# Optimization experiments

Measured on AMD Instinct MI355X. Metric: run time of the kernel, lower is better.

The kernel has to match this reference:

```python
import jax, jax.numpy as jnp
import numpy as np
from jax import lax

DROPOUT = 0.6  # input dropout rate (recurrent_dropout = 0.0)


def _lstm_layer(x, Wk, Wr, b, drop_key, rate):
    """Keras-style LSTM (gate order i,f,c,o) with per-gate time-constant input dropout.
    x: [B,T,D]; Wk: [D,4U]; Wr: [U,4U]; b: [4U]. Returns (hs [B,T,U], h_last [B,U])."""
    B, T, D = x.shape
    U = Wr.shape[0]
    Wk4 = Wk.reshape(D, 4, U)
    Wr4 = Wr.reshape(U, 4, U)
    b4 = b.reshape(4, U)
    if rate > 0.0:
        keep = 1.0 - rate
        masks = jax.random.bernoulli(drop_key, keep, (4, B, D)).astype(x.dtype) / keep
    else:
        masks = jnp.ones((4, B, D), dtype=x.dtype)

    def step(carry, x_t):
        h, c = carry
        # per-gate dropped inputs: [4,B,D] -> [B,4,U]
        z = jnp.einsum('gbd,dgu->bgu', x_t[None] * masks, Wk4)
        z = z + jnp.einsum('bu,ugv->bgv', h, Wr4) + b4
        i = jax.nn.sigmoid(z[:, 0])
        f = jax.nn.sigmoid(z[:, 1])
        g = jnp.tanh(z[:, 2])
        o = jax.nn.sigmoid(z[:, 3])
        c = f * c + i * g
        h = o * jnp.tanh(c)
        return (h, c), h

    h0 = jnp.zeros((B, U), dtype=x.dtype)
    c0 = jnp.zeros((B, U), dtype=x.dtype)
    (h_last, _), hs = lax.scan(step, (h0, c0), x.transpose(1, 0, 2))
    return hs.transpose(1, 0, 2), h_last


def _glorot(key, shape):
    fan_in, fan_out = shape[0], shape[1]
    scale = jnp.sqrt(2.0 / (fan_in + fan_out)).astype(jnp.float32)
    return jax.random.normal(key, shape, dtype=jnp.float32) * scale


def setup_inputs() -> dict:
    key = jax.random.key(0)
    B, T, D, H, L = 256, 1024, 128, 128, 64
    ks = jax.random.split(key, 10)
    x = jax.random.normal(ks[0], (B, T, D), dtype=jnp.float32)
    return {
        'x': x,
        'Wk0': _glorot(ks[1], (D, 4 * H)), 'Wr0': _glorot(ks[2], (H, 4 * H)),
        'b0': jnp.zeros((4 * H,), jnp.float32),
        'Wk1': _glorot(ks[3], (H, 4 * H)), 'Wr1': _glorot(ks[4], (H, 4 * H)),
        'b1': jnp.zeros((4 * H,), jnp.float32),
        'Wko': _glorot(ks[5], (H, 4 * L)), 'Wro': _glorot(ks[6], (L, 4 * L)),
        'bo': jnp.zeros((4 * L,), jnp.float32),
    }


def reference(x, Wk0, Wr0, b0, Wk1, Wr1, b1, Wko, Wro, bo):
    dk = jax.random.split(jax.random.key(4347), 3)
    h, _ = _lstm_layer(x, Wk0, Wr0, b0, dk[0], DROPOUT)      # hidden layer 0, return_sequences
    h, _ = _lstm_layer(h, Wk1, Wr1, b1, dk[1], DROPOUT)      # hidden layer 1, return_sequences
    _, h_last = _lstm_layer(h, Wko, Wro, bo, dk[2], DROPOUT)  # output layer, last state only
    return h_last
```

## Files before the change

### kernel.cpp

```cpp
#include <hip/hip_runtime.h>
#include <hip/hip_bf16.h>
#include <hip/hip_fp16.h>
#include <stdint.h>


#define MODE_F32  0
#define MODE_F16  2

typedef _Float16 f16x8 __attribute__((ext_vector_type(8)));
typedef float    f32x4 __attribute__((ext_vector_type(4)));

__device__ __forceinline__ float h16f(uint16_t b){
  __half_raw hr; hr.x = b; return __half2float(__half(hr));
}

__device__ __forceinline__ float fexp2(float x){
#if __has_builtin(__builtin_amdgcn_exp2f)
  return __builtin_amdgcn_exp2f(x);
#else
  return exp2f(x);
#endif
}
__device__ __forceinline__ float frcp(float x){
#if __has_builtin(__builtin_amdgcn_rcpf)
  return __builtin_amdgcn_rcpf(x);
#else
  return 1.0f/x;
#endif
}
#define LOG2E  1.4426950408889634f
#define LOG2E2 2.8853900817779268f

template<int M>
__device__ __forceinline__ void cvt8(const void* p, size_t i, float* o){
  if constexpr (M == MODE_F32){
    const float* f = (const float*)p + i;
    float4 a = *(const float4*)f;
    float4 b = *(const float4*)(f + 4);
    o[0]=a.x; o[1]=a.y; o[2]=a.z; o[3]=a.w;
    o[4]=b.x; o[5]=b.y; o[6]=b.z; o[7]=b.w;
  } else {
    uint4 r = *(const uint4*)((const uint16_t*)p + i);
    uint32_t hw[4] = {r.x, r.y, r.z, r.w};
    #pragma unroll
    for (int q=0;q<4;q++){
      o[2*q]   = h16f((uint16_t)(hw[q] & 0xffffu));
      o[2*q+1] = h16f((uint16_t)(hw[q] >> 16));
    }
  }
}

__device__ __forceinline__ void tf2x32(uint32_t k0, uint32_t k1,
                                       uint32_t& x0, uint32_t& x1){
  uint32_t ks2 = k0 ^ k1 ^ 0x1BD11BDAu;
  x0 += k0; x1 += k1;
#define TF_R(r) { x0 += x1; x1 = (x1<<r)|(x1>>(32-r)); x1 ^= x0; }
  TF_R(13) TF_R(15) TF_R(26) TF_R(6)  x0 += k1;  x1 += ks2 + 1u;
  TF_R(17) TF_R(29) TF_R(16) TF_R(24) x0 += ks2; x1 += k0  + 2u;
  TF_R(13) TF_R(15) TF_R(26) TF_R(6)  x0 += k0;  x1 += k1  + 3u;
  TF_R(17) TF_R(29) TF_R(16) TF_R(24) x0 += k1;  x1 += ks2 + 4u;
  TF_R(13) TF_R(15) TF_R(26) TF_R(6)  x0 += ks2; x1 += k0  + 5u;
#undef TF_R
}

__device__ __forceinline__ float bern_mask(uint32_t bits){
  float u = __uint_as_float((bits >> 9) | 0x3f800000u) - 1.0f;
  return (u < 0.4f) ? 2.5f : 0.0f;
}

__global__ void mask_kernel(float* __restrict__ masks){
  int gid = blockIdx.x * 256 + threadIdx.x;
  int layer = gid >> 17;
  uint32_t i = (uint32_t)(gid & 131071);
  uint32_t k0 = 0u, k1 = (uint32_t)layer;
  tf2x32(0u, 4347u, k0, k1);
  uint32_t x0 = 0u, x1 = i;
  tf2x32(k0, k1, x0, x1);
  masks[gid] = bern_mask(x0 ^ x1);
}

template<int U, int AM>
__global__ __launch_bounds__(256) void gemm_mfma(
    const void*  __restrict__ A,
    const float* __restrict__ W,
    const float* __restrict__ bias,
    const float* __restrict__ maskL,
    __half* __restrict__ Z)
{
  constexpr int WC   = 4*U;
  constexpr int HALF = U/2;
  __shared__ _Float16 As [128][128];
  __shared__ _Float16 Bst[U  ][128];
  const int tid  = threadIdx.x;
  const int r0   = blockIdx.x * 128;
  const int gate = blockIdx.y;
  const int bb   = blockIdx.x >> 3;
  const float* mrow = maskL + gate*32768 + bb*128;

  {
    const int r  = tid >> 1;
    const int kh = (tid & 1) * 64;
    #pragma unroll
    for (int c=0;c<8;c++){
      int k0 = kh + c*8;
      float av[8]; cvt8<AM>(A, (size_t)(r0+r)*128 + k0, av);
      float4 m0 = *(const float4*)(mrow+k0);
      float4 m1 = *(const float4*)(mrow+k0+4);
      _Float16* dst = &As[r][k0 ^ ((r&7)<<3)];
      dst[0]=(_Float16)(av[0]*m0.x); dst[1]=(_Float16)(av[1]*m0.y);
      dst[2]=(_Float16)(av[2]*m0.z); dst[3]=(_Float16)(av[3]*m0.w);
      dst[4]=(_Float16)(av[4]*m1.x); dst[5]=(_Float16)(av[5]*m1.y);
      dst[6]=(_Float16)(av[6]*m1.z); dst[7]=(_Float16)(av[7]*m1.w);
    }
  }
  {
    const int d  = tid >> 1;
    const int ch = (tid & 1) * HALF;
    #pragma unroll
    for (int cc=0; cc<HALF/8; ++cc){
      int c0 = ch + cc*8;
      const float* wp = W + (size_t)d*WC + gate*U + c0;
      float4 w0 = *(const float4*)wp;
      float4 w1 = *(const float4*)(wp+4);
      float wv[8] = {w0.x,w0.y,w0.z,w0.w,w1.x,w1.y,w1.z,w1.w};
      #pragma unroll
      for (int q=0;q<8;q++){
        int c = c0 + q;
        Bst[c][d ^ ((c&7)<<3)] = (_Float16)wv[q];
      }
    }
  }
  __syncthreads();

  const int l  = tid & 63;
  const int w  = tid >> 6;
  const int lr = l & 15;
  const int kg = (l >> 4) * 8;
  constexpr int MF = (U==128) ? 4 : 2;
  const int wr = (U==128) ? ((w>>1)*64) : (w*32);
  const int wc = (U==128) ? ((w&1)*64) : 0;

  f32x4 zz = {0.f,0.f,0.f,0.f};
  f32x4 acc[MF][4];
  #pragma unroll
  for (int m=0;m<MF;m++)
    #pragma unroll
    for (int n=0;n<4;n++) acc[m][n] = zz;

  #pragma unroll
  for (int ks=0; ks<4; ++ks){
    const int kb = ks*32 + kg;
    f16x8 af[MF], bf[4];
    #pragma unroll
    for (int m=0;m<MF;m++){
      int r = wr + m*16 + lr;
      af[m] = *(const f16x8*)&As[r][kb ^ ((r&7)<<3)];
    }
    #pragma unroll
    for (int n=0;n<4;n++){
      int c = wc + n*16 + lr;
      bf[n] = *(const f16x8*)&Bst[c][kb ^ ((c&7)<<3)];
    }
    #pragma unroll
    for (int m=0;m<MF;m++)
      #pragma unroll
      for (int n=0;n<4;n++)
        acc[m][n] = __builtin_amdgcn_mfma_f32_16x16x32_f16(af[m], bf[n], acc[m][n], 0, 0, 0);
  }

  const int crow = (l>>4)*4;
  float bv[4];
  #pragma unroll
  for (int n=0;n<4;n++) bv[n] = bias[gate*U + wc + n*16 + lr];
  #pragma unroll
  for (int m=0;m<MF;m++){
    #pragma unroll
    for (int n=0;n<4;n++){
      int cc = wc + n*16 + lr;
      #pragma unroll
      for (int j=0;j<4;j++){
        int rr = wr + m*16 + crow + j;
        Z[(size_t)(r0+rr)*WC + gate*U + cc] = __float2half(acc[m][n][j] + bv[n]);
      }
    }
  }
}

template<int U, bool SEQ, int VAR>
__global__ __launch_bounds__(4*U, 1) void rec5_kernel(
    const __half* __restrict__ Zin,
    const float*  __restrict__ Wr,
    __half* __restrict__ Hseq,
    float*  __restrict__ Hlast)
{
  constexpr int C   = 4*U;
  constexpr int KS  = U/32;
  constexpr int TS  = 32;
  constexpr int TBH = TS*C;
  constexpr int NCH = 4;
  const int row = blockIdx.x;
  const int tid = threadIdx.x;
  const int l   = tid & 63;
  const int w   = tid >> 6;
  const int lr  = l & 15;
  const int kg  = (l >> 4) * 8;
  const int u   = w*16 + lr;

  __shared__ _Float16 zt[2][TBH];
  __shared__ _Float16 hbuf[2][U];

  f16x8 bf[4][KS];
  #pragma unroll
  for (int g=0; g<4; ++g)
    #pragma unroll
    for (int ks=0; ks<KS; ++ks)
      #pragma unroll
      for (int j=0; j<8; ++j)
        bf[g][ks][j] = (_Float16)Wr[(size_t)(ks*32 + kg + j)*C + g*U + u];

  if (tid < U) hbuf[0][tid] = (_Float16)0.0f;
  float cst = 0.0f;

  const char* zrow = (const char*)Zin + (size_t)row*1024*C*2;
  auto stage = [&](int tile, int buf){
    const char* gsrc = zrow + (size_t)tile*TBH*2;
    char* lbase = (char*)&zt[buf][0];
    #pragma unroll
    for (int c=0; c<NCH; ++c){
      int off = c*(4*U*16) + tid*16;
      __builtin_amdgcn_global_load_lds(
          (const uint32_t*)(gsrc + off),
          (uint32_t*)(lbase + c*(4*U*16) + w*1024),
          16, 0, 0);
    }
  };
  stage(0, 0);

  uint16_t* hsq = nullptr;
  if constexpr (SEQ) hsq = (uint16_t*)Hseq + (size_t)row*1024*U + u;

  asm volatile("s_waitcnt vmcnt(0) lgkmcnt(0)" ::: "memory");
  __builtin_amdgcn_s_barrier();

  for (int tile=0; tile<1024/TS; ++tile){
    const int buf = tile & 1;
    if (tile+1 < 1024/TS) stage(tile+1, buf^1);

    #pragma unroll 1
    for (int s8=0; s8<TS/8; ++s8){
      uint16_t hr[8];
      #pragma unroll
      for (int r8=0; r8<8; ++r8){
        const int s  = s8*8 + r8;
        const int tt = tile*TS + s;
        const int hb = r8 & 1;
        f16x8 af[KS];
        #pragma unroll
        for (int ks=0; ks<KS; ++ks)
          af[ks] = *(const f16x8*)&hbuf[hb][ks*32 + kg];
        float zg0 = (float)zt[buf][s*C         + u];
        float zg1 = (float)zt[buf][s*C +   U   + u];
        float zg2 = (float)zt[buf][s*C + 2*U   + u];
        float zg3 = (float)zt[buf][s*C + 3*U   + u];
        f32x4 acc[4];
        acc[0] = (f32x4){zg0,zg0,zg0,zg0};
        acc[1] = (f32x4){zg1,zg1,zg1,zg1};
        acc[2] = (f32x4){zg2,zg2,zg2,zg2};
        acc[3] = (f32x4){zg3,zg3,zg3,zg3};
        #pragma unroll
        for (int g=0; g<4; ++g)
          #pragma unroll
          for (int ks=0; ks<KS; ++ks)
            acc[g] = __builtin_amdgcn_mfma_f32_16x16x32_f16(af[ks], bf[g][ks], acc[g], 0, 0, 0);
        float gi = frcp(1.0f + fexp2(-LOG2E * acc[0][0]));
        float gf = frcp(1.0f + fexp2(-LOG2E * acc[1][0]));
        float gg = 1.0f - 2.0f*frcp(fexp2(LOG2E2 * acc[2][0]) + 1.0f);
        float go = frcp(1.0f + fexp2(-LOG2E * acc[3][0]));
        cst = fmaf(gf, cst, gi*gg);
        float h = go * (1.0f - 2.0f*frcp(fexp2(LOG2E2 * cst) + 1.0f));
        __half hh = __float2half(h);
        hr[r8] = *(uint16_t*)&hh;
        if (l < 16){
          hbuf[hb ^ 1][u] = *(_Float16*)&hh;
          if constexpr (!SEQ){
            if (tt == 1023) Hlast[(size_t)row*U + u] = h;
          }
        }
        if constexpr (VAR == 0){
          __builtin_amdgcn_sched_barrier(0);
          asm volatile("s_waitcnt lgkmcnt(0)");
          __builtin_amdgcn_s_barrier();
          __builtin_amdgcn_sched_barrier(0);
        } else {
          asm volatile("s_waitcnt lgkmcnt(0)\n\ts_barrier" ::: "memory");
        }
      }
      if constexpr (SEQ){
        if (l < 16){
          uint16_t* hp = hsq + (size_t)(tile*TS + s8*8)*U;
          #pragma unroll
          for (int j=0; j<8; ++j) hp[(size_t)j*U] = hr[j];
        }
      }
    }
    if (tile+1 < 1024/TS){
      asm volatile("s_waitcnt vmcnt(0)" ::: "memory");
      __builtin_amdgcn_s_barrier();
    }
  }
}

extern "C" void kernel_launch(void* const* d_in, const int* in_sizes, int n_in,
                              void* d_out, int out_size, void* d_ws, size_t ws_size,
                              hipStream_t stream)
{
  (void)in_sizes; (void)n_in; (void)out_size; (void)ws_size;
  const void*  x   = d_in[0];
  const float* Wk0 = (const float*)d_in[1];
  const float* Wr0 = (const float*)d_in[2];
  const float* b0  = (const float*)d_in[3];
  const float* Wk1 = (const float*)d_in[4];
  const float* Wr1 = (const float*)d_in[5];
  const float* b1  = (const float*)d_in[6];
  const float* Wko = (const float*)d_in[7];
  const float* Wro = (const float*)d_in[8];
  const float* bo  = (const float*)d_in[9];

  char* ws = (char*)d_ws;
  float*  masks = (float*)(ws + 256);
  __half* zin   = (__half*)(ws + 256 + 3*131072*4);
  __half* h0    = (__half*)((char*)zin + (size_t)262144*512*2);
  __half* h1    = h0 + (size_t)262144*128;
  float*  out   = (float*)d_out;

  mask_kernel<<<1536, 256, 0, stream>>>(masks);

  gemm_mfma<128, MODE_F32><<<dim3(2048,4), 256, 0, stream>>>(x, Wk0, b0, masks, zin);
  rec5_kernel<128, true, 0><<<256, 512, 0, stream>>>(zin, Wr0, (__half*)h0, nullptr);
  gemm_mfma<128, MODE_F16><<<dim3(2048,4), 256, 0, stream>>>(h0, Wk1, b1, masks + 131072, zin);
  rec5_kernel<128, true, 1><<<256, 512, 0, stream>>>(zin, Wr1, (__half*)h1, nullptr);
  gemm_mfma<64, MODE_F16><<<dim3(2048,4), 256, 0, stream>>>(h1, Wko, bo, masks + 262144, zin);
  rec5_kernel<64, false, 1><<<256, 256, 0, stream>>>(zin, Wro, nullptr, out);
}
```

Before: 1.861 ms.

## Halve recurrent block size: each wave computes two 16-column hidden slices

The recurrent LSTM kernel now launches half as many threads per batch row, and each wave owns two 16-unit column blocks with two sets of register-resident recurrent weights and two cell states. Halving the wave count aims to cut per-timestep barrier cost across the block, and the two independent MFMA chains can interleave to hide latency. The cost is twice the MFMA and activation work per wave on the serial critical path, higher register pressure, and twice the staging loads per thread.

```diff
diff --git a/kernel.cpp b/kernel.cpp
--- a/kernel.cpp
+++ b/kernel.cpp
@@ -30,6 +30,13 @@
 }
 #define LOG2E  1.4426950408889634f
 #define LOG2E2 2.8853900817779268f
+
+__device__ __forceinline__ float fsig(float x){
+  return frcp(1.0f + fexp2(-LOG2E * x));
+}
+__device__ __forceinline__ float ftanh(float x){
+  return 1.0f - 2.0f*frcp(fexp2(LOG2E2 * x) + 1.0f);
+}
 
 template<int M>
 __device__ __forceinline__ void cvt8(const void* p, size_t i, float* o){
@@ -186,8 +193,8 @@
   }
 }
 
-template<int U, bool SEQ, int VAR>
-__global__ __launch_bounds__(4*U, 1) void rec5_kernel(
+template<int U, bool SEQ>
+__global__ __launch_bounds__(2*U, 1) void rec6_kernel(
     const __half* __restrict__ Zin,
     const float*  __restrict__ Wr,
     __half* __restrict__ Hseq,
@@ -197,29 +204,32 @@
   constexpr int KS  = U/32;
   constexpr int TS  = 32;
   constexpr int TBH = TS*C;
-  constexpr int NCH = 4;
+  constexpr int NCH = 8;
   const int row = blockIdx.x;
   const int tid = threadIdx.x;
   const int l   = tid & 63;
   const int w   = tid >> 6;
   const int lr  = l & 15;
   const int kg  = (l >> 4) * 8;
-  const int u   = w*16 + lr;
+  const int u0  = w*32 + lr;
+  const int u1  = u0 + 16;
 
   __shared__ _Float16 zt[2][TBH];
   __shared__ _Float16 hbuf[2][U];
 
-  f16x8 bf[4][KS];
-  #pragma unroll
-  for (int g=0; g<4; ++g)
-    #pragma unroll
-    for (int ks=0; ks<KS; ++ks)
-      #pragma unroll
-      for (int j=0; j<8; ++j)
-        bf[g][ks][j] = (_Float16)Wr[(size_t)(ks*32 + kg + j)*C + g*U + u];
+  f16x8 bf[2][4][KS];
+  #pragma unroll
+  for (int cb=0; cb<2; ++cb)
+    #pragma unroll
+    for (int g=0; g<4; ++g)
+      #pragma unroll
+      for (int ks=0; ks<KS; ++ks)
+        #pragma unroll
+        for (int j=0; j<8; ++j)
+          bf[cb][g][ks][j] = (_Float16)Wr[(size_t)(ks*32 + kg + j)*C + g*U + u0 + cb*16];
 
   if (tid < U) hbuf[0][tid] = (_Float16)0.0f;
-  float cst = 0.0f;
+  float cstA = 0.0f, cstB = 0.0f;
 
   const char* zrow = (const char*)Zin + (size_t)row*1024*C*2;
   auto stage = [&](int tile, int buf){
@@ -227,17 +237,17 @@
     char* lbase = (char*)&zt[buf][0];
     #pragma unroll
     for (int c=0; c<NCH; ++c){
-      int off = c*(4*U*16) + tid*16;
+      int off = c*(2*U*16) + tid*16;
       __builtin_amdgcn_global_load_lds(
           (const uint32_t*)(gsrc + off),
-          (uint32_t*)(lbase + c*(4*U*16) + w*1024),
+          (uint32_t*)(lbase + c*(2*U*16) + w*1024),
           16, 0, 0);
     }
   };
   stage(0, 0);
 
   uint16_t* hsq = nullptr;
-  if constexpr (SEQ) hsq = (uint16_t*)Hseq + (size_t)row*1024*U + u;
+  if constexpr (SEQ) hsq = (uint16_t*)Hseq + (size_t)row*1024*U;
 
   asm volatile("s_waitcnt vmcnt(0) lgkmcnt(0)" ::: "memory");
   __builtin_amdgcn_s_barrier();
@@ -248,7 +258,7 @@
 
     #pragma unroll 1
     for (int s8=0; s8<TS/8; ++s8){
-      uint16_t hr[8];
+      uint16_t hrA[8], hrB[8];
       #pragma unroll
       for (int r8=0; r8<8; ++r8){
         const int s  = s8*8 + r8;
@@ -258,48 +268,61 @@
         #pragma unroll
         for (int ks=0; ks<KS; ++ks)
           af[ks] = *(const f16x8*)&hbuf[hb][ks*32 + kg];
-        float zg0 = (float)zt[buf][s*C         + u];
-        float zg1 = (float)zt[buf][s*C +   U   + u];
-        float zg2 = (float)zt[buf][s*C + 2*U   + u];
-        float zg3 = (float)zt[buf][s*C + 3*U   + u];
-        f32x4 acc[4];
-        acc[0] = (f32x4){zg0,zg0,zg0,zg0};
-        acc[1] = (f32x4){zg1,zg1,zg1,zg1};
-        acc[2] = (f32x4){zg2,zg2,zg2,zg2};
-        acc[3] = (f32x4){zg3,zg3,zg3,zg3};
+        float zg[2][4];
+        #pragma unroll
+        for (int cb=0; cb<2; ++cb)
+          #pragma unroll
+          for (int g=0; g<4; ++g)
+            zg[cb][g] = (float)zt[buf][s*C + g*U + u0 + cb*16];
+        f32x4 accA[4], accB[4];
+        #pragma unroll
+        for (int g=0; g<4; ++g){
+          accA[g] = (f32x4){zg[0][g], zg[0][g], zg[0][g], zg[0][g]};
+          accB[g] = (f32x4){zg[1][g], zg[1][g], zg[1][g], zg[1][g]};
+        }
         #pragma unroll
         for (int g=0; g<4; ++g)
           #pragma unroll
-          for (int ks=0; ks<KS; ++ks)
-            acc[g] = __builtin_amdgcn_mfma_f32_16x16x32_f16(af[ks], bf[g][ks], acc[g], 0, 0, 0);
-        float gi = frcp(1.0f + fexp2(-LOG2E * acc[0][0]));
-        float gf = frcp(1.0f + fexp2(-LOG2E * acc[1][0]));
-        float gg = 1.0f - 2.0f*frcp(fexp2(LOG2E2 * acc[2][0]) + 1.0f);
-        float go = frcp(1.0f + fexp2(-LOG2E * acc[3][0]));
-        cst = fmaf(gf, cst, gi*gg);
-        float h = go * (1.0f - 2.0f*frcp(fexp2(LOG2E2 * cst) + 1.0f));
-        __half hh = __float2half(h);
-        hr[r8] = *(uint16_t*)&hh;
+          for (int ks=0; ks<KS; ++ks){
+            accA[g] = __builtin_amdgcn_mfma_f32_16x16x32_f16(af[ks], bf[0][g][ks], accA[g], 0, 0, 0);
+            accB[g] = __builtin_amdgcn_mfma_f32_16x16x32_f16(af[ks], bf[1][g][ks], accB[g], 0, 0, 0);
+          }
+        float hA, hB;
+        {
+          float gi = fsig(accA[0][0]), gf = fsig(accA[1][0]);
+          float gg = ftanh(accA[2][0]), go = fsig(accA[3][0]);
+          cstA = fmaf(gf, cstA, gi*gg);
+          hA = go * ftanh(cstA);
+        }
+        {
+          float gi = fsig(accB[0][0]), gf = fsig(accB[1][0]);
+          float gg = ftanh(accB[2][0]), go = fsig(accB[3][0]);
+          cstB = fmaf(gf, cstB, gi*gg);
+          hB = go * ftanh(cstB);
+        }
+        __half hhA = __float2half(hA), hhB = __float2half(hB);
+        hrA[r8] = *(uint16_t*)&hhA;
+        hrB[r8] = *(uint16_t*)&hhB;
         if (l < 16){
-          hbuf[hb ^ 1][u] = *(_Float16*)&hh;
+          hbuf[hb ^ 1][u0] = *(_Float16*)&hhA;
+          hbuf[hb ^ 1][u1] = *(_Float16*)&hhB;
           if constexpr (!SEQ){
-            if (tt == 1023) Hlast[(size_t)row*U + u] = h;
+            if (tt == 1023){
+              Hlast[(size_t)row*U + u0] = hA;
+              Hlast[(size_t)row*U + u1] = hB;
+            }
           }
         }
-        if constexpr (VAR == 0){
-          __builtin_amdgcn_sched_barrier(0);
-          asm volatile("s_waitcnt lgkmcnt(0)");
-          __builtin_amdgcn_s_barrier();
-          __builtin_amdgcn_sched_barrier(0);
-        } else {
-          asm volatile("s_waitcnt lgkmcnt(0)\n\ts_barrier" ::: "memory");
-        }
+        asm volatile("s_waitcnt lgkmcnt(0)\n\ts_barrier" ::: "memory");
       }
       if constexpr (SEQ){
         if (l < 16){
           uint16_t* hp = hsq + (size_t)(tile*TS + s8*8)*U;
           #pragma unroll
-          for (int j=0; j<8; ++j) hp[(size_t)j*U] = hr[j];
+          for (int j=0; j<8; ++j){
+            hp[(size_t)j*U + u0] = hrA[j];
+            hp[(size_t)j*U + u1] = hrB[j];
+          }
         }
       }
     }
@@ -336,9 +359,9 @@
   mask_kernel<<<1536, 256, 0, stream>>>(masks);
 
   gemm_mfma<128, MODE_F32><<<dim3(2048,4), 256, 0, stream>>>(x, Wk0, b0, masks, zin);
-  rec5_kernel<128, true, 0><<<256, 512, 0, stream>>>(zin, Wr0, (__half*)h0, nullptr);
+  rec6_kernel<128, true><<<256, 256, 0, stream>>>(zin, Wr0, (__half*)h0, nullptr);
   gemm_mfma<128, MODE_F16><<<dim3(2048,4), 256, 0, stream>>>(h0, Wk1, b1, masks + 131072, zin);
-  rec5_kernel<128, true, 1><<<256, 512, 0, stream>>>(zin, Wr1, (__half*)h1, nullptr);
+  rec6_kernel<128, true><<<256, 256, 0, stream>>>(zin, Wr1, (__half*)h1, nullptr);
   gemm_mfma<64, MODE_F16><<<dim3(2048,4), 256, 0, stream>>>(h1, Wko, bo, masks + 262144, zin);
-  rec5_kernel<64, false, 1><<<256, 256, 0, stream>>>(zin, Wro, nullptr, out);
-}
+  rec6_kernel<64, false><<<256, 128, 0, stream>>>(zin, Wro, nullptr, out);
+}
```

After: 2.268 ms. 21.9% more time.
